# Performance work log

Hardware: AMD Instinct MI355X
Metric: run time of the kernel (lower is better)

Reference implementation:

```python
import jax, jax.numpy as jnp
import numpy as np

T, B, A, H = 256, 64, 8, 512


def setup_inputs() -> dict:
    key = jax.random.key(0)
    k0, k1, k2, k3, k4, k5 = jax.random.split(key, 6)
    ins = jax.random.normal(k0, (T, B, A, H), dtype=jnp.float32)
    resets = jax.random.randint(k1, (T, B, A), 0, 2) > 0  # episode-reset flags
    scale = 1.0 / np.sqrt(H).astype(np.float32)
    # Flax GRUCell params: input dense ir/iz/in (with bias) concatenated -> Wi, bi;
    # hidden dense hr/hz (no bias) and hn (bias bhn) concatenated -> Wh, bhn.
    Wi = jax.random.normal(k2, (H, 3 * H), dtype=jnp.float32) * scale
    bi = jax.random.normal(k3, (3 * H,), dtype=jnp.float32) * 0.01
    Wh = jax.random.normal(k4, (H, 3 * H), dtype=jnp.float32) * scale
    bhn = jax.random.normal(k5, (H,), dtype=jnp.float32) * 0.01
    return {"ins": ins, "resets": resets, "Wi": Wi, "bi": bi, "Wh": Wh, "bhn": bhn}


def reference(ins, resets, Wi, bi, Wh, bhn):
    # ins: [T, B, A, H], resets: [T, B, A] bool
    Tn, Bn, An, Hn = ins.shape
    # Precompute all input-side gate projections in one big GEMM: [T,B,A,3H]
    x_gates = jnp.einsum("tbah,hg->tbag", ins, Wi) + bi

    def step(h, inp):
        xg_t, reset_t = inp  # xg_t: [B,A,3H], reset_t: [B,A]
        hg = jnp.einsum("bah,hg->bag", h, Wh)  # [B,A,3H]
        xr, xz, xn = jnp.split(xg_t, 3, axis=-1)
        hr, hz, hn = jnp.split(hg, 3, axis=-1)
        r = jax.nn.sigmoid(xr + hr)
        z = jax.nn.sigmoid(xz + hz)
        n = jnp.tanh(xn + r * (hn + bhn))
        new_h = (1.0 - z) * n + z * h  # GRUCell output (pre-reset)
        # Reset masking applies to the carry only, not to the emitted output.
        carry = jnp.where(reset_t[..., None], jnp.zeros_like(new_h), new_h)
        return carry, new_h

    h0 = jnp.zeros((Bn, An, Hn), dtype=ins.dtype)  # initialize_carry -> zeros
    _, ys = jax.lax.scan(step, h0, (x_gates, resets))
    return ys  # [T, B, A, H]
```

## Files before the change

### kernel.cpp

```cpp
#include <hip/hip_runtime.h>
#include <hip/hip_fp16.h>


#define T_STEPS 256
#define NCELL   512
#define HD      512
#define G3      1536

typedef _Float16 f16;
typedef _Float16 half8   __attribute__((ext_vector_type(8)));
typedef float    floatx16 __attribute__((ext_vector_type(16)));
typedef float    float4v  __attribute__((ext_vector_type(4)));
typedef unsigned long long u64;

#define PACKS_ELEMS (16 * 6 * 32 * 64 * 8)
#define HBUF_OFF    (PACKS_ELEMS * 2)
#define HBUF_ELEMS  (NCELL * HD)
#define CNT_OFF     (HBUF_OFF + 2 * HBUF_ELEMS * 2)

__global__ void pack_weights(const float* __restrict__ Wi,
                             const float* __restrict__ Wh,
                             f16* __restrict__ packs) {
    int idx = blockIdx.x * blockDim.x + threadIdx.x;
    if (idx >= PACKS_ELEMS) return;
    int j  = idx & 7;
    int l  = (idx >> 3) & 63;
    int it = (idx >> 9) & 31;
    int s  = (idx >> 14) % 6;
    int ng = idx / (6 << 14);
    int k    = it * 16 + (l >> 5) * 8 + j;
    int gcol = (s % 3) * 512 + ng * 32 + (l & 31);
    const float* W = (s < 3) ? Wi : Wh;
    packs[idx] = (f16)W[(size_t)k * G3 + gcol];
}

__launch_bounds__(256, 1)
__global__ void gru_scan(const float* __restrict__ ins,
                         const int*   __restrict__ resets,
                         const float* __restrict__ bi,
                         const float* __restrict__ bhn,
                         const f16*   __restrict__ packs,
                         f16*         __restrict__ hbuf,
                         int*         __restrict__ flags,
                         float*       __restrict__ out) {
    __shared__ float red[4][4][4][64][4];

    const int bid  = blockIdx.x;
    const int xcd  = bid & 7;
    const int rest = bid >> 3;
    const int ng   = rest & 15;
    const int mg   = xcd + 8 * (rest >> 4);
    const int tid  = threadIdx.x;
    const int lane = tid & 63;
    const int w    = tid >> 6;
    const int lm   = lane & 31;
    const int lh   = lane >> 5;

    half8 bw[6][8];
    {
        const half8* p = (const half8*)packs;
#pragma unroll
        for (int s = 0; s < 6; ++s)
#pragma unroll
            for (int itl = 0; itl < 8; ++itl)
                bw[s][itl] = p[((ng * 6 + s) * 32 + (w * 8 + itl)) * 64 + lane];
    }

    const int col0 = ng * 32 + lm;
    const float bir = bi[col0], biz = bi[512 + col0], bin = bi[1024 + col0];
    const float bhv = bhn[col0];

    const int cell_a = mg * 32 + lm;
    const int kbase  = w * 128 + lh * 8;
    const int row0   = 8 * w + 4 * lh;
    const f16* hb0 = hbuf;
    const f16* hb1 = hbuf + HBUF_ELEMS;
    int* myflags = flags + mg * 32;

    float hprev[4];
#pragma unroll
    for (int el = 0; el < 4; ++el) hprev[el] = 0.f;

    float4v xa[8], xb[8];
    {
        const float* xr0 = ins + (size_t)cell_a * HD + kbase;
#pragma unroll
        for (int itl = 0; itl < 8; ++itl) {
            const float4v* px = (const float4v*)(xr0 + itl * 16);
            xa[itl] = px[0];
            xb[itl] = px[1];
        }
    }
    half8 xf[8];
#pragma unroll
    for (int itl = 0; itl < 8; ++itl) {
        half8 v;
#pragma unroll
        for (int e = 0; e < 4; ++e) { v[e] = (f16)xa[itl][e]; v[4 + e] = (f16)xb[itl][e]; }
        xf[itl] = v;
    }

    for (int t = 0; t < T_STEPS; ++t) {
        const f16* hr_ = (t & 1) ? hb1 : hb0;
        f16*       hw_ = (f16*)((t & 1) ? hb0 : hb1);

        floatx16 ar, az, anx, anh;
#pragma unroll
        for (int i = 0; i < 16; ++i) { ar[i] = 0.f; az[i] = 0.f; anx[i] = 0.f; anh[i] = 0.f; }
#pragma unroll
        for (int itl = 0; itl < 8; ++itl) {
            ar  = __builtin_amdgcn_mfma_f32_32x32x16_f16(xf[itl], bw[0][itl], ar,  0, 0, 0);
            az  = __builtin_amdgcn_mfma_f32_32x32x16_f16(xf[itl], bw[1][itl], az,  0, 0, 0);
            anx = __builtin_amdgcn_mfma_f32_32x32x16_f16(xf[itl], bw[2][itl], anx, 0, 0, 0);
        }

        {
            int tn = (t + 1 < T_STEPS) ? (t + 1) : t;
            const float* xrn = ins + ((size_t)tn * NCELL + cell_a) * HD + kbase;
#pragma unroll
            for (int itl = 0; itl < 8; ++itl) {
                const float4v* px = (const float4v*)(xrn + itl * 16);
                xa[itl] = px[0];
                xb[itl] = px[1];
            }
        }

        for (;;) {
            int v = __hip_atomic_load(&myflags[lane & 15], __ATOMIC_RELAXED,
                                      __HIP_MEMORY_SCOPE_AGENT);
            if (!__any(v < t)) break;
        }
        asm volatile("" ::: "memory");

        half8 hf[8];
        {
            const u64* hsrc = (const u64*)(hr_ + (size_t)cell_a * HD + kbase);
#pragma unroll
            for (int itl = 0; itl < 8; ++itl) {
                union { u64 q[2]; half8 v; } u;
                u.q[0] = __hip_atomic_load(hsrc + itl * 4 + 0, __ATOMIC_RELAXED,
                                           __HIP_MEMORY_SCOPE_AGENT);
                u.q[1] = __hip_atomic_load(hsrc + itl * 4 + 1, __ATOMIC_RELAXED,
                                           __HIP_MEMORY_SCOPE_AGENT);
                hf[itl] = u.v;
            }
        }

#pragma unroll
        for (int itl = 0; itl < 8; ++itl) {
            ar  = __builtin_amdgcn_mfma_f32_32x32x16_f16(hf[itl], bw[3][itl], ar,  0, 0, 0);
            az  = __builtin_amdgcn_mfma_f32_32x32x16_f16(hf[itl], bw[4][itl], az,  0, 0, 0);
            anh = __builtin_amdgcn_mfma_f32_32x32x16_f16(hf[itl], bw[5][itl], anh, 0, 0, 0);
        }

#pragma unroll
        for (int q = 0; q < 4; ++q) {
            float4v v;
            v[0] = ar[4*q]; v[1] = ar[4*q+1]; v[2] = ar[4*q+2]; v[3] = ar[4*q+3];
            *(float4v*)&red[w][0][q][lane][0] = v;
            v[0] = az[4*q]; v[1] = az[4*q+1]; v[2] = az[4*q+2]; v[3] = az[4*q+3];
            *(float4v*)&red[w][1][q][lane][0] = v;
            v[0] = anx[4*q]; v[1] = anx[4*q+1]; v[2] = anx[4*q+2]; v[3] = anx[4*q+3];
            *(float4v*)&red[w][2][q][lane][0] = v;
            v[0] = anh[4*q]; v[1] = anh[4*q+1]; v[2] = anh[4*q+2]; v[3] = anh[4*q+3];
            *(float4v*)&red[w][3][q][lane][0] = v;
        }
        {
            half8 xfn[8];
#pragma unroll
            for (int itl = 0; itl < 8; ++itl) {
                half8 v;
#pragma unroll
                for (int e = 0; e < 4; ++e) { v[e] = (f16)xa[itl][e]; v[4 + e] = (f16)xb[itl][e]; }
                xfn[itl] = v;
            }
#pragma unroll
            for (int itl = 0; itl < 8; ++itl) xf[itl] = xfn[itl];
        }
        __syncthreads();

        float rr[4], rz[4], rnx[4], rnh[4];
#pragma unroll
        for (int el = 0; el < 4; ++el) { rr[el] = 0.f; rz[el] = 0.f; rnx[el] = 0.f; rnh[el] = 0.f; }
#pragma unroll
        for (int ww = 0; ww < 4; ++ww) {
            float4v v0 = *(const float4v*)&red[ww][0][w][lane][0];
            float4v v1 = *(const float4v*)&red[ww][1][w][lane][0];
            float4v v2 = *(const float4v*)&red[ww][2][w][lane][0];
            float4v v3 = *(const float4v*)&red[ww][3][w][lane][0];
#pragma unroll
            for (int el = 0; el < 4; ++el) {
                rr[el]  += v0[el];
                rz[el]  += v1[el];
                rnx[el] += v2[el];
                rnh[el] += v3[el];
            }
        }

#pragma unroll
        for (int el = 0; el < 4; ++el) {
            int cell = mg * 32 + row0 + el;
            float var = rr[el]  + bir;
            float vaz = rz[el]  + biz;
            float vnx = rnx[el] + bin;
            float vnh = rnh[el] + bhv;
            float r = 1.0f / (1.0f + __expf(-var));
            float z = 1.0f / (1.0f + __expf(-vaz));
            float hp = hprev[el];
            float narg = vnx + r * vnh;
            narg = fminf(fmaxf(narg, -30.f), 30.f);
            float ex = __expf(2.f * narg);
            float n  = (ex - 1.f) / (ex + 1.f);
            float nh = (1.f - z) * n + z * hp;
            out[((size_t)t * NCELL + cell) * HD + col0] = nh;
            int rs = resets[t * NCELL + cell];
            float carry = rs ? 0.f : nh;
            hprev[el] = carry;
            union { unsigned short s; f16 h; } cv; cv.h = (f16)carry;
            __hip_atomic_store((unsigned short*)&hw_[(size_t)cell * HD + col0],
                               cv.s, __ATOMIC_RELAXED, __HIP_MEMORY_SCOPE_AGENT);
        }

        __syncthreads();
        if (tid == 0) {
            __hip_atomic_store(&myflags[ng], t + 1, __ATOMIC_RELAXED,
                               __HIP_MEMORY_SCOPE_AGENT);
        }
    }
}

extern "C" void kernel_launch(void* const* d_in, const int* in_sizes, int n_in,
                              void* d_out, int out_size, void* d_ws, size_t ws_size,
                              hipStream_t stream) {
    const float* ins    = (const float*)d_in[0];
    const int*   resets = (const int*)  d_in[1];
    const float* Wi     = (const float*)d_in[2];
    const float* bi     = (const float*)d_in[3];
    const float* Wh     = (const float*)d_in[4];
    const float* bhn    = (const float*)d_in[5];
    float* out = (float*)d_out;

    char* ws = (char*)d_ws;
    f16* packs = (f16*)ws;
    f16* hbuf  = (f16*)(ws + HBUF_OFF);
    int* flags = (int*)(ws + CNT_OFF);

    hipMemsetAsync(ws + HBUF_OFF, 0, (size_t)2 * HBUF_ELEMS * 2 + 4096, stream);

    pack_weights<<<(PACKS_ELEMS + 255) / 256, 256, 0, stream>>>(Wi, Wh, packs);
    gru_scan<<<256, 256, 0, stream>>>(ins, resets, bi, bhn, packs, hbuf, flags, out);
}
```

Measured before the change: 1.990 ms.

## Bind row groups to XCDs at runtime and use XCD-local L2 coherence for sync

Each block reads its hardware XCC id and takes a slot from a per-XCC atomic counter. It then maps itself so that all 16 column-group blocks sharing a row group land on the same XCD. With that placement guaranteed, the hidden-state and flag exchange uses sc0 loads, plain stores and a workgroup-scope flag store instead of agent-scope atomics. The goal is to keep the per-timestep handoff inside one XCD's L2 and avoid device-wide coherence latency. This relies on exactly 32 blocks being resident per XCD and on L2 visibility for the weaker memory ordering. A dummy LDS pad is added to the shared-memory footprint.

```diff
diff --git a/kernel.cpp b/kernel.cpp
--- a/kernel.cpp
+++ b/kernel.cpp
@@ -41,21 +41,29 @@
                          const float* __restrict__ bhn,
                          const f16*   __restrict__ packs,
                          f16*         __restrict__ hbuf,
-                         int*         __restrict__ flags,
+                         int*         __restrict__ sync,
                          float*       __restrict__ out) {
     __shared__ float red[4][4][4][64][4];
-
-    const int bid  = blockIdx.x;
-    const int xcd  = bid & 7;
-    const int rest = bid >> 3;
-    const int ng   = rest & 15;
-    const int mg   = xcd + 8 * (rest >> 4);
+    __shared__ int   lds_pad[5120];
+    __shared__ int   slot_sh;
+
     const int tid  = threadIdx.x;
     const int lane = tid & 63;
     const int w    = tid >> 6;
     const int lm   = lane & 31;
     const int lh   = lane >> 5;
 
+    int xcc;
+    asm volatile("s_getreg_b32 %0, hwreg(HW_REG_XCC_ID, 0, 32)" : "=s"(xcc));
+    xcc &= 7;
+    if (tid == 0)
+        slot_sh = atomicAdd(&sync[512 + xcc], 1);
+    __syncthreads();
+    const int slot = slot_sh;
+    if (slot == 0x7fffffff) lds_pad[tid] = tid;
+    const int ng = slot & 15;
+    const int mg = xcc * 2 + ((slot >> 4) & 1);
+
     half8 bw[6][8];
     {
         const half8* p = (const half8*)packs;
@@ -75,7 +83,8 @@
     const int row0   = 8 * w + 4 * lh;
     const f16* hb0 = hbuf;
     const f16* hb1 = hbuf + HBUF_ELEMS;
-    int* myflags = flags + mg * 32;
+    int* myflags = sync + mg * 32;
+    const int* fladdr = &myflags[lane & 15];
 
     float hprev[4];
 #pragma unroll
@@ -126,24 +135,23 @@
         }
 
         for (;;) {
-            int v = __hip_atomic_load(&myflags[lane & 15], __ATOMIC_RELAXED,
-                                      __HIP_MEMORY_SCOPE_AGENT);
+            int v;
+            asm volatile("global_load_dword %0, %1, off sc0\n\t"
+                         "s_waitcnt vmcnt(0)"
+                         : "=v"(v) : "v"(fladdr) : "memory");
             if (!__any(v < t)) break;
         }
-        asm volatile("" ::: "memory");
 
         half8 hf[8];
         {
-            const u64* hsrc = (const u64*)(hr_ + (size_t)cell_a * HD + kbase);
+            const f16* hbase = hr_ + (size_t)cell_a * HD + kbase;
 #pragma unroll
             for (int itl = 0; itl < 8; ++itl) {
-                union { u64 q[2]; half8 v; } u;
-                u.q[0] = __hip_atomic_load(hsrc + itl * 4 + 0, __ATOMIC_RELAXED,
-                                           __HIP_MEMORY_SCOPE_AGENT);
-                u.q[1] = __hip_atomic_load(hsrc + itl * 4 + 1, __ATOMIC_RELAXED,
-                                           __HIP_MEMORY_SCOPE_AGENT);
-                hf[itl] = u.v;
-            }
+                asm volatile("global_load_dwordx4 %0, %1, off sc0"
+                             : "=v"(hf[itl]) : "v"(hbase + itl * 16) : "memory");
+            }
+            asm volatile("s_waitcnt vmcnt(0)" ::: "memory");
+            __builtin_amdgcn_sched_barrier(0);
         }
 
 #pragma unroll
@@ -216,15 +224,13 @@
             int rs = resets[t * NCELL + cell];
             float carry = rs ? 0.f : nh;
             hprev[el] = carry;
-            union { unsigned short s; f16 h; } cv; cv.h = (f16)carry;
-            __hip_atomic_store((unsigned short*)&hw_[(size_t)cell * HD + col0],
-                               cv.s, __ATOMIC_RELAXED, __HIP_MEMORY_SCOPE_AGENT);
+            hw_[(size_t)cell * HD + col0] = (f16)carry;
         }
 
         __syncthreads();
         if (tid == 0) {
             __hip_atomic_store(&myflags[ng], t + 1, __ATOMIC_RELAXED,
-                               __HIP_MEMORY_SCOPE_AGENT);
+                               __HIP_MEMORY_SCOPE_WORKGROUP);
         }
     }
 }
@@ -243,10 +249,10 @@
     char* ws = (char*)d_ws;
     f16* packs = (f16*)ws;
     f16* hbuf  = (f16*)(ws + HBUF_OFF);
-    int* flags = (int*)(ws + CNT_OFF);
+    int* syncp = (int*)(ws + CNT_OFF);
 
     hipMemsetAsync(ws + HBUF_OFF, 0, (size_t)2 * HBUF_ELEMS * 2 + 4096, stream);
 
     pack_weights<<<(PACKS_ELEMS + 255) / 256, 256, 0, stream>>>(Wi, Wh, packs);
-    gru_scan<<<256, 256, 0, stream>>>(ins, resets, bi, bhn, packs, hbuf, flags, out);
+    gru_scan<<<256, 256, 0, stream>>>(ins, resets, bi, bhn, packs, hbuf, syncp, out);
 }
```

Result: faster. 1.708 ms (-14.2%).
